# Kernel tuning notes

Measured on AMD Instinct MI355X. Metric: run time of the kernel, lower is better.

## Reference

```python
import jax, jax.numpy as jnp
import numpy as np

N_NODES = 100000


def gcn_conv(x, src, dst, W, b):
    # x: [N, F_in]; src/dst include self-loops; symmetric degree normalization (PyG GCNConv)
    n = x.shape[0]
    xw = x @ W  # [N, F_out]
    ones = jnp.ones(dst.shape[0], dtype=xw.dtype)
    deg = jax.ops.segment_sum(ones, dst, num_segments=n)  # in-degree incl. self-loop
    dinv = jnp.where(deg > 0, jax.lax.rsqrt(deg), 0.0)
    norm = dinv[src] * dinv[dst]  # [E]
    msg = xw[src] * norm[:, None]  # gather + per-edge scale
    out = jax.ops.segment_sum(msg, dst, num_segments=n)  # scatter-add aggregation
    return out + b


def setup_inputs() -> dict:
    key = jax.random.key(0)
    ks = jax.random.split(key, 6)
    F_in = 512
    E = 3200000
    x = jax.random.normal(ks[0], (N_NODES, F_in), dtype=jnp.float32)
    edge_index = jax.random.randint(ks[1], (2, E), 0, N_NODES, dtype=jnp.int64)
    W1 = jax.random.normal(ks[2], (F_in, 16), dtype=jnp.float32) * (1.0 / np.sqrt(F_in))
    b1 = jnp.zeros((16,), dtype=jnp.float32)
    W2 = jax.random.normal(ks[3], (16, 16), dtype=jnp.float32) * 0.25
    b2 = jnp.zeros((16,), dtype=jnp.float32)
    fc_w = jax.random.normal(ks[4], (16, 1), dtype=jnp.float32) * 0.25
    fc_b = jnp.zeros((1,), dtype=jnp.float32)
    return {"x": x, "edge_index": edge_index, "W1": W1, "b1": b1,
            "W2": W2, "b2": b2, "fc_w": fc_w, "fc_b": fc_b}


def reference(x, edge_index, W1, b1, W2, b2, fc_w, fc_b):
    n = x.shape[0]
    loop = jnp.arange(n, dtype=edge_index.dtype)
    src = jnp.concatenate([edge_index[0], loop])  # add self-loops
    dst = jnp.concatenate([edge_index[1], loop])
    h = jax.nn.relu(gcn_conv(x, src, dst, W1, b1))
    h = jax.nn.relu(gcn_conv(h, src, dst, W2, b2))
    g = jnp.mean(h, axis=0, keepdims=True)  # global_mean_pool, single graph -> [1, 16]
    return g @ fc_w + fc_b  # [1, 1]
```

## Files before the change

kernel.cpp:

```cpp
#include <hip/hip_runtime.h>
#include <stdint.h>

#define F_IN 512
#define F_OUT 16
#define CB_SHIFT 8
#define CB_W 256
#define PER 6250
#define SORT_CAP 6400

__device__ inline float4 f4_shfl_xor(float4 v, int mask) {
    float4 r;
    r.x = __shfl_xor(v.x, mask);
    r.y = __shfl_xor(v.y, mask);
    r.z = __shfl_xor(v.z, mask);
    r.w = __shfl_xor(v.w, mask);
    return r;
}

__global__ __launch_bounds__(256) void k_chist(const int* __restrict__ ei, int E, int K1, int B,
                                               int* __restrict__ cntT) {
    __shared__ int h[512];
    int t = threadIdx.x;
    for (int i = t; i < K1; i += 256) h[i] = 0;
    __syncthreads();
    int e0 = blockIdx.x * PER, e1 = min(E, e0 + PER);
    for (int e = e0 + t; e < e1; e += 256)
        atomicAdd(&h[ei[(size_t)E + e] >> CB_SHIFT], 1);
    __syncthreads();
    for (int i = t; i < K1; i += 256) cntT[(size_t)i * B + blockIdx.x] = h[i];
}

__global__ __launch_bounds__(512) void k_btot(const int* __restrict__ cntT, int B, int K1,
                                              int* __restrict__ bucketBase, int* __restrict__ bucketCnt) {
    __shared__ int sm[512];
    int k = threadIdx.x;
    int tot = 0;
    if (k < K1) {
        const int4* row = (const int4*)(cntT + (size_t)k * B);
        for (int b = 0; b < B / 4; b++) {
            int4 v = row[b];
            tot += v.x + v.y + v.z + v.w;
        }
    }
    sm[k] = tot;
    __syncthreads();
    for (int off = 1; off < 512; off <<= 1) {
        int add = (k >= off) ? sm[k - off] : 0;
        __syncthreads();
        sm[k] += add;
        __syncthreads();
    }
    if (k < K1) { bucketBase[k] = sm[k] - tot; bucketCnt[k] = tot; }
}

__global__ __launch_bounds__(512) void k_bbase(const int* __restrict__ cntT, int B,
                                               const int* __restrict__ bucketBase,
                                               int* __restrict__ baseT) {
    __shared__ int sm[512];
    int k = blockIdx.x, t = threadIdx.x;
    int v = (t < B) ? cntT[(size_t)k * B + t] : 0;
    sm[t] = v;
    __syncthreads();
    for (int off = 1; off < 512; off <<= 1) {
        int add = (t >= off) ? sm[t - off] : 0;
        __syncthreads();
        sm[t] += add;
        __syncthreads();
    }
    if (t < B) baseT[(size_t)k * B + t] = bucketBase[k] + sm[t] - v;
}

__global__ __launch_bounds__(512) void k_csort(const int* __restrict__ ei, int E, int K1, int B,
                                               const int* __restrict__ baseT, unsigned* __restrict__ part) {
    __shared__ unsigned sorted[SORT_CAP];
    __shared__ int h[512], lb[512], cur[512], gb[512];
    int t = threadIdx.x;
    int e0 = blockIdx.x * PER, e1 = min(E, e0 + PER);
    int C = e1 - e0;
    h[t] = 0;
    __syncthreads();
    for (int e = e0 + t; e < e1; e += 512)
        atomicAdd(&h[ei[(size_t)E + e] >> CB_SHIFT], 1);
    __syncthreads();
    int v = h[t];
    lb[t] = v;
    __syncthreads();
    for (int off = 1; off < 512; off <<= 1) {
        int add = (t >= off) ? lb[t - off] : 0;
        __syncthreads();
        lb[t] += add;
        __syncthreads();
    }
    int excl = lb[t] - v;
    __syncthreads();
    lb[t] = excl;
    cur[t] = excl;
    if (t < K1) gb[t] = baseT[(size_t)t * B + blockIdx.x];
    __syncthreads();
    for (int e = e0 + t; e < e1; e += 512) {
        int s = ei[e];
        int d = ei[(size_t)E + e];
        int pos = atomicAdd(&cur[d >> CB_SHIFT], 1);
        sorted[pos] = ((unsigned)s << CB_SHIFT) | (unsigned)(d & (CB_W - 1));
    }
    __syncthreads();
    int wv = t >> 6, ln = t & 63;
    for (int k = wv; k < K1; k += 8) {
        int s0 = lb[k];
        int s1 = cur[k];
        int g  = gb[k];
        for (int i = s0 + ln; i < s1; i += 64)
            part[(size_t)g + (i - s0)] = sorted[i];
    }
}

__global__ __launch_bounds__(512) void k_prep2(const unsigned* __restrict__ part,
                                               const int* __restrict__ bucketBase, const int* __restrict__ bucketCnt,
                                               int* __restrict__ hist, float* __restrict__ dinv,
                                               int* __restrict__ offsets, int* __restrict__ csr, int N) {
    __shared__ int fh[CB_W], fb[CB_W], cur[CB_W];
    int k = blockIdx.x, t = threadIdx.x;
    int base = bucketBase[k], cnt = bucketCnt[k];
    int d0 = k << CB_SHIFT;
    if (t < CB_W) fh[t] = 0;
    __syncthreads();
    for (int i = t; i < cnt; i += 512)
        atomicAdd(&fh[part[(size_t)base + i] & (CB_W - 1)], 1);
    __syncthreads();
    int v = 0;
    if (t < CB_W) { v = fh[t]; fb[t] = v; }
    __syncthreads();
    for (int off = 1; off < CB_W; off <<= 1) {
        int add = (t >= off && t < CB_W) ? fb[t - off] : 0;
        __syncthreads();
        if (t < CB_W) fb[t] += add;
        __syncthreads();
    }
    if (t < CB_W) {
        int excl = fb[t] - v;
        int n = d0 + t;
        if (n < N) {
            offsets[n] = base + excl;
            hist[n] = v;
            dinv[n] = rsqrtf((float)(v + 1));
        }
        cur[t] = excl;
    }
    __syncthreads();
    for (int i = t; i < cnt; i += 512) {
        unsigned e = part[(size_t)base + i];
        int pos = atomicAdd(&cur[e & (CB_W - 1)], 1);
        csr[(size_t)base + pos] = (int)(e >> CB_SHIFT);
    }
}

__global__ __launch_bounds__(128) void k_gemm1(const float* __restrict__ x, const float* __restrict__ W1,
                                               const float* __restrict__ dinv, float* __restrict__ xw1p, int N) {
    __shared__ float4 Wv[2048];
    const float4* w1v = (const float4*)W1;
    for (int i = threadIdx.x; i < 2048; i += 128) Wv[i] = w1v[i];
    __syncthreads();

    int t = threadIdx.x;
    int n0 = blockIdx.x * 256 + t;
    int n1 = n0 + 128;
    const float4* xr0 = (const float4*)(x + (size_t)min(n0, N - 1) * F_IN);
    const float4* xr1 = (const float4*)(x + (size_t)min(n1, N - 1) * F_IN);

    float acc0[16], acc1[16];
#pragma unroll
    for (int j = 0; j < 16; j++) { acc0[j] = 0.f; acc1[j] = 0.f; }

#pragma unroll 2
    for (int kk = 0; kk < 128; kk++) {
        float4 x0 = xr0[kk];
        float4 x1 = xr1[kk];
        const float4* wr = &Wv[kk * 16];
#pragma unroll
        for (int i = 0; i < 4; i++) {
            float xs0 = (i == 0) ? x0.x : (i == 1) ? x0.y : (i == 2) ? x0.z : x0.w;
            float xs1 = (i == 0) ? x1.x : (i == 1) ? x1.y : (i == 2) ? x1.z : x1.w;
#pragma unroll
            for (int q = 0; q < 4; q++) {
                float4 wv = wr[i * 4 + q];
                acc0[q*4+0] = fmaf(xs0, wv.x, acc0[q*4+0]);
                acc0[q*4+1] = fmaf(xs0, wv.y, acc0[q*4+1]);
                acc0[q*4+2] = fmaf(xs0, wv.z, acc0[q*4+2]);
                acc0[q*4+3] = fmaf(xs0, wv.w, acc0[q*4+3]);
                acc1[q*4+0] = fmaf(xs1, wv.x, acc1[q*4+0]);
                acc1[q*4+1] = fmaf(xs1, wv.y, acc1[q*4+1]);
                acc1[q*4+2] = fmaf(xs1, wv.z, acc1[q*4+2]);
                acc1[q*4+3] = fmaf(xs1, wv.w, acc1[q*4+3]);
            }
        }
    }
    if (n0 < N) {
        float dn = dinv[n0];
        float4* orow = (float4*)(xw1p + (size_t)n0 * F_OUT);
#pragma unroll
        for (int q = 0; q < 4; q++)
            orow[q] = make_float4(dn*acc0[q*4+0], dn*acc0[q*4+1], dn*acc0[q*4+2], dn*acc0[q*4+3]);
    }
    if (n1 < N) {
        float dn = dinv[n1];
        float4* orow = (float4*)(xw1p + (size_t)n1 * F_OUT);
#pragma unroll
        for (int q = 0; q < 4; q++)
            orow[q] = make_float4(dn*acc1[q*4+0], dn*acc1[q*4+1], dn*acc1[q*4+2], dn*acc1[q*4+3]);
    }
}

__global__ __launch_bounds__(256) void k_agg1(const float* __restrict__ xw, const int* __restrict__ offsets,
                                              const int* __restrict__ hist, const float* __restrict__ dinv,
                                              const int* __restrict__ csr, const float* __restrict__ b1,
                                              const float* __restrict__ W2, float* __restrict__ xw2p, int N) {
    __shared__ float W2s[256];
    if (threadIdx.x < 256) W2s[threadIdx.x] = W2[threadIdx.x];
    __syncthreads();

    int lane = threadIdx.x & 63;
    int wave = threadIdx.x >> 6;
    int grp  = lane >> 4;
    int sub  = lane & 15;
    int eo   = sub >> 2;
    int q    = sub & 3;
    int node = blockIdx.x * 16 + wave * 4 + grp;
    if (node >= N) return;

    int start = offsets[node], cnt = hist[node];
    float dn = dinv[node];
    float4 a0 = make_float4(0.f,0.f,0.f,0.f), a1 = a0, a2 = a0, a3 = a0;
    int i = 0;
    for (; i + 16 <= cnt; i += 16) {
        int s0 = csr[start + i + eo];
        int s1 = csr[start + i + 4 + eo];
        int s2 = csr[start + i + 8 + eo];
        int s3 = csr[start + i + 12 + eo];
        float4 v0 = ((const float4*)(xw + (size_t)s0 * F_OUT))[q];
        float4 v1 = ((const float4*)(xw + (size_t)s1 * F_OUT))[q];
        float4 v2 = ((const float4*)(xw + (size_t)s2 * F_OUT))[q];
        float4 v3 = ((const float4*)(xw + (size_t)s3 * F_OUT))[q];
        a0.x+=v0.x; a0.y+=v0.y; a0.z+=v0.z; a0.w+=v0.w;
        a1.x+=v1.x; a1.y+=v1.y; a1.z+=v1.z; a1.w+=v1.w;
        a2.x+=v2.x; a2.y+=v2.y; a2.z+=v2.z; a2.w+=v2.w;
        a3.x+=v3.x; a3.y+=v3.y; a3.z+=v3.z; a3.w+=v3.w;
    }
    for (; i + 8 <= cnt; i += 8) {
        int s0 = csr[start + i + eo];
        int s1 = csr[start + i + 4 + eo];
        float4 v0 = ((const float4*)(xw + (size_t)s0 * F_OUT))[q];
        float4 v1 = ((const float4*)(xw + (size_t)s1 * F_OUT))[q];
        a0.x+=v0.x; a0.y+=v0.y; a0.z+=v0.z; a0.w+=v0.w;
        a1.x+=v1.x; a1.y+=v1.y; a1.z+=v1.z; a1.w+=v1.w;
    }
    for (; i < cnt; i += 4) {
        if (i + eo < cnt) {
            int s0 = csr[start + i + eo];
            float4 v0 = ((const float4*)(xw + (size_t)s0 * F_OUT))[q];
            a0.x+=v0.x; a0.y+=v0.y; a0.z+=v0.z; a0.w+=v0.w;
        }
    }
    float4 acc;
    acc.x = a0.x+a1.x+a2.x+a3.x;
    acc.y = a0.y+a1.y+a2.y+a3.y;
    acc.z = a0.z+a1.z+a2.z+a3.z;
    acc.w = a0.w+a1.w+a2.w+a3.w;
    { float4 u = f4_shfl_xor(acc, 4); acc.x+=u.x; acc.y+=u.y; acc.z+=u.z; acc.w+=u.w; }
    { float4 u = f4_shfl_xor(acc, 8); acc.x+=u.x; acc.y+=u.y; acc.z+=u.z; acc.w+=u.w; }

    float4 sv = ((const float4*)(xw + (size_t)node * F_OUT))[q];
    float4 bq = ((const float4*)b1)[q];
    float4 h;
    h.x = fmaxf(dn * (acc.x + sv.x) + bq.x, 0.f);
    h.y = fmaxf(dn * (acc.y + sv.y) + bq.y, 0.f);
    h.z = fmaxf(dn * (acc.z + sv.z) + bq.z, 0.f);
    h.w = fmaxf(dn * (acc.w + sv.w) + bq.w, 0.f);

    float o = 0.f;
#pragma unroll
    for (int a = 0; a < 4; a++) {
        int src = (grp << 4) + a;
        float h0 = __shfl(h.x, src);
        float h1 = __shfl(h.y, src);
        float h2 = __shfl(h.z, src);
        float h3 = __shfl(h.w, src);
        o += h0 * W2s[(a*4+0)*16 + sub] + h1 * W2s[(a*4+1)*16 + sub]
           + h2 * W2s[(a*4+2)*16 + sub] + h3 * W2s[(a*4+3)*16 + sub];
    }
    xw2p[(size_t)node * F_OUT + sub] = dn * o;
}

__global__ __launch_bounds__(256) void k_agg2(const float* __restrict__ xw, const int* __restrict__ offsets,
                                              const int* __restrict__ hist, const float* __restrict__ dinv,
                                              const int* __restrict__ csr, const float* __restrict__ b2,
                                              float* __restrict__ partials, int N) {
    int lane = threadIdx.x & 63;
    int wave = threadIdx.x >> 6;
    int grp  = lane >> 4;
    int sub  = lane & 15;
    int eo   = sub >> 2;
    int q    = sub & 3;
    int node = blockIdx.x * 16 + wave * 4 + grp;

    float4 m = make_float4(0.f, 0.f, 0.f, 0.f);
    if (node < N) {
        int start = offsets[node], cnt = hist[node];
        float dn = dinv[node];
        float4 a0 = make_float4(0.f,0.f,0.f,0.f), a1 = a0, a2 = a0, a3 = a0;
        int i = 0;
        for (; i + 16 <= cnt; i += 16) {
            int s0 = csr[start + i + eo];
            int s1 = csr[start + i + 4 + eo];
            int s2 = csr[start + i + 8 + eo];
            int s3 = csr[start + i + 12 + eo];
            float4 v0 = ((const float4*)(xw + (size_t)s0 * F_OUT))[q];
            float4 v1 = ((const float4*)(xw + (size_t)s1 * F_OUT))[q];
            float4 v2 = ((const float4*)(xw + (size_t)s2 * F_OUT))[q];
            float4 v3 = ((const float4*)(xw + (size_t)s3 * F_OUT))[q];
            a0.x+=v0.x; a0.y+=v0.y; a0.z+=v0.z; a0.w+=v0.w;
            a1.x+=v1.x; a1.y+=v1.y; a1.z+=v1.z; a1.w+=v1.w;
            a2.x+=v2.x; a2.y+=v2.y; a2.z+=v2.z; a2.w+=v2.w;
            a3.x+=v3.x; a3.y+=v3.y; a3.z+=v3.z; a3.w+=v3.w;
        }
        for (; i + 8 <= cnt; i += 8) {
            int s0 = csr[start + i + eo];
            int s1 = csr[start + i + 4 + eo];
            float4 v0 = ((const float4*)(xw + (size_t)s0 * F_OUT))[q];
            float4 v1 = ((const float4*)(xw + (size_t)s1 * F_OUT))[q];
            a0.x+=v0.x; a0.y+=v0.y; a0.z+=v0.z; a0.w+=v0.w;
            a1.x+=v1.x; a1.y+=v1.y; a1.z+=v1.z; a1.w+=v1.w;
        }
        for (; i < cnt; i += 4) {
            if (i + eo < cnt) {
                int s0 = csr[start + i + eo];
                float4 v0 = ((const float4*)(xw + (size_t)s0 * F_OUT))[q];
                a0.x+=v0.x; a0.y+=v0.y; a0.z+=v0.z; a0.w+=v0.w;
            }
        }
        float4 acc;
        acc.x = a0.x+a1.x+a2.x+a3.x;
        acc.y = a0.y+a1.y+a2.y+a3.y;
        acc.z = a0.z+a1.z+a2.z+a3.z;
        acc.w = a0.w+a1.w+a2.w+a3.w;
        { float4 u = f4_shfl_xor(acc, 4); acc.x+=u.x; acc.y+=u.y; acc.z+=u.z; acc.w+=u.w; }
        { float4 u = f4_shfl_xor(acc, 8); acc.x+=u.x; acc.y+=u.y; acc.z+=u.z; acc.w+=u.w; }
        float4 sv = ((const float4*)(xw + (size_t)node * F_OUT))[q];
        float4 bq = ((const float4*)b2)[q];
        if (eo == 0) {
            m.x = fmaxf(dn * (acc.x + sv.x) + bq.x, 0.f);
            m.y = fmaxf(dn * (acc.y + sv.y) + bq.y, 0.f);
            m.z = fmaxf(dn * (acc.z + sv.z) + bq.z, 0.f);
            m.w = fmaxf(dn * (acc.w + sv.w) + bq.w, 0.f);
        }
    }
    { float4 u = f4_shfl_xor(m, 16); m.x+=u.x; m.y+=u.y; m.z+=u.z; m.w+=u.w; }
    { float4 u = f4_shfl_xor(m, 32); m.x+=u.x; m.y+=u.y; m.z+=u.z; m.w+=u.w; }
    __shared__ float smf[4][16];
    if (lane < 4) {
        smf[wave][q*4+0] = m.x;
        smf[wave][q*4+1] = m.y;
        smf[wave][q*4+2] = m.z;
        smf[wave][q*4+3] = m.w;
    }
    __syncthreads();
    if (threadIdx.x < 16) {
        float s = smf[0][threadIdx.x] + smf[1][threadIdx.x] + smf[2][threadIdx.x] + smf[3][threadIdx.x];
        partials[(size_t)blockIdx.x * 16 + threadIdx.x] = s;
    }
}

__global__ void k_final(const float* __restrict__ partials, int NB, const float* __restrict__ fc_w,
                        const float* __restrict__ fc_b, float* __restrict__ out, float invN) {
    __shared__ float sm[64][16];
    int t = threadIdx.x;
    int g = t >> 4, j = t & 15;
    float s = 0.0f;
    for (int bk = g; bk < NB; bk += 64) s += partials[(size_t)bk * 16 + j];
    sm[g][j] = s;
    __syncthreads();
    for (int str = 32; str > 0; str >>= 1) {
        if (g < str) sm[g][j] += sm[g + str][j];
        __syncthreads();
    }
    if (t == 0) {
        float acc = fc_b[0];
#pragma unroll
        for (int jj = 0; jj < 16; jj++) acc += sm[0][jj] * invN * fc_w[jj];
        out[0] = acc;
    }
}

extern "C" void kernel_launch(void* const* d_in, const int* in_sizes, int n_in,
                              void* d_out, int out_size, void* d_ws, size_t ws_size,
                              hipStream_t stream) {
    const float* x   = (const float*)d_in[0];
    const int*   ei  = (const int*)d_in[1];
    const float* W1  = (const float*)d_in[2];
    const float* b1  = (const float*)d_in[3];
    const float* W2  = (const float*)d_in[4];
    const float* b2  = (const float*)d_in[5];
    const float* fcw = (const float*)d_in[6];
    const float* fcb = (const float*)d_in[7];
    float* out = (float*)d_out;

    int N = in_sizes[0] / F_IN;
    int E = in_sizes[1] / 2;
    int K1 = (N + CB_W - 1) >> CB_SHIFT;
    int B1 = (E + PER - 1) / PER;

    char* p = (char*)d_ws;
    auto alloc = [&](size_t bytes) {
        void* r = (void*)p;
        p += (bytes + 255) & ~(size_t)255;
        return r;
    };
    int*   cntT       = (int*)alloc((size_t)K1 * B1 * 4);
    int*   baseT      = (int*)alloc((size_t)K1 * B1 * 4);
    int*   bucketBase = (int*)alloc((size_t)K1 * 4);
    int*   bucketCnt  = (int*)alloc((size_t)K1 * 4);
    int*   hist       = (int*)alloc((size_t)N * 4);
    int*   offsets    = (int*)alloc((size_t)N * 4);
    float* dinv       = (float*)alloc((size_t)N * 4);
    int*   csr        = (int*)alloc((size_t)E * 4);
    unsigned* part    = (unsigned*)alloc((size_t)E * 4);
    int NB_NODE = (N + 15) / 16;
    float* partials = (float*)alloc((size_t)NB_NODE * 16 * 4);
    float* xw1p = (float*)part;
    float* xw2p = xw1p + (size_t)N * F_OUT;

    k_chist<<<B1, 256, 0, stream>>>(ei, E, K1, B1, cntT);
    k_btot<<<1, 512, 0, stream>>>(cntT, B1, K1, bucketBase, bucketCnt);
    k_bbase<<<K1, 512, 0, stream>>>(cntT, B1, bucketBase, baseT);
    k_csort<<<B1, 512, 0, stream>>>(ei, E, K1, B1, baseT, part);
    k_prep2<<<K1, 512, 0, stream>>>(part, bucketBase, bucketCnt, hist, dinv, offsets, csr, N);

    k_gemm1<<<(N + 255) / 256, 128, 0, stream>>>(x, W1, dinv, xw1p, N);
    k_agg1<<<NB_NODE, 256, 0, stream>>>(xw1p, offsets, hist, dinv, csr, b1, W2, xw2p, N);
    k_agg2<<<NB_NODE, 256, 0, stream>>>(xw2p, offsets, hist, dinv, csr, b2, partials, N);
    k_final<<<1, 1024, 0, stream>>>(partials, NB_NODE, fcw, fcb, out, 1.0f / (float)N);
}
```

Baseline: 258.6 us.

## Simplify GEMM1 to one row per thread, widen csort copy groups, deepen agg unroll

The first-layer GEMM now gives each of 256 threads a single row and reads W1 directly from global memory (uniform addresses, likely scalar or broadcast loads) instead of staging it in LDS with two rows per thread. The csort scatter-out loop uses 16-lane groups per bucket instead of whole 64-lane waves, which suits short per-bucket runs. Both aggregation kernels gain a 32-edge unrolled loop so each lane has eight independent gathers in flight. The changes trade LDS reuse and per-thread work for more threads and memory-level parallelism, at some cost in register pressure.

```diff
diff --git a/kernel.cpp b/kernel.cpp
--- a/kernel.cpp
+++ b/kernel.cpp
@@ -76,7 +76,6 @@
     __shared__ int h[512], lb[512], cur[512], gb[512];
     int t = threadIdx.x;
     int e0 = blockIdx.x * PER, e1 = min(E, e0 + PER);
-    int C = e1 - e0;
     h[t] = 0;
     __syncthreads();
     for (int e = e0 + t; e < e1; e += 512)
@@ -104,12 +103,12 @@
         sorted[pos] = ((unsigned)s << CB_SHIFT) | (unsigned)(d & (CB_W - 1));
     }
     __syncthreads();
-    int wv = t >> 6, ln = t & 63;
-    for (int k = wv; k < K1; k += 8) {
+    int g16 = t >> 4, ln = t & 15;
+    for (int k = g16; k < K1; k += 32) {
         int s0 = lb[k];
         int s1 = cur[k];
         int g  = gb[k];
-        for (int i = s0 + ln; i < s1; i += 64)
+        for (int i = s0 + ln; i < s1; i += 16)
             part[(size_t)g + (i - s0)] = sorted[i];
     }
 }
@@ -154,60 +153,38 @@
     }
 }
 
-__global__ __launch_bounds__(128) void k_gemm1(const float* __restrict__ x, const float* __restrict__ W1,
+__global__ __launch_bounds__(256) void k_gemm1(const float* __restrict__ x, const float* __restrict__ W1,
                                                const float* __restrict__ dinv, float* __restrict__ xw1p, int N) {
-    __shared__ float4 Wv[2048];
-    const float4* w1v = (const float4*)W1;
-    for (int i = threadIdx.x; i < 2048; i += 128) Wv[i] = w1v[i];
-    __syncthreads();
-
-    int t = threadIdx.x;
-    int n0 = blockIdx.x * 256 + t;
-    int n1 = n0 + 128;
-    const float4* xr0 = (const float4*)(x + (size_t)min(n0, N - 1) * F_IN);
-    const float4* xr1 = (const float4*)(x + (size_t)min(n1, N - 1) * F_IN);
-
-    float acc0[16], acc1[16];
-#pragma unroll
-    for (int j = 0; j < 16; j++) { acc0[j] = 0.f; acc1[j] = 0.f; }
-
-#pragma unroll 2
+    int n = blockIdx.x * 256 + threadIdx.x;
+    if (n >= N) return;
+    const float4* xr = (const float4*)(x + (size_t)n * F_IN);
+    const float4* wr = (const float4*)W1;
+
+    float acc[16];
+#pragma unroll
+    for (int j = 0; j < 16; j++) acc[j] = 0.f;
+
+#pragma unroll 4
     for (int kk = 0; kk < 128; kk++) {
-        float4 x0 = xr0[kk];
-        float4 x1 = xr1[kk];
-        const float4* wr = &Wv[kk * 16];
+        float4 xv = xr[kk];
 #pragma unroll
         for (int i = 0; i < 4; i++) {
-            float xs0 = (i == 0) ? x0.x : (i == 1) ? x0.y : (i == 2) ? x0.z : x0.w;
-            float xs1 = (i == 0) ? x1.x : (i == 1) ? x1.y : (i == 2) ? x1.z : x1.w;
+            float xs = (i == 0) ? xv.x : (i == 1) ? xv.y : (i == 2) ? xv.z : xv.w;
 #pragma unroll
             for (int q = 0; q < 4; q++) {
-                float4 wv = wr[i * 4 + q];
-                acc0[q*4+0] = fmaf(xs0, wv.x, acc0[q*4+0]);
-                acc0[q*4+1] = fmaf(xs0, wv.y, acc0[q*4+1]);
-                acc0[q*4+2] = fmaf(xs0, wv.z, acc0[q*4+2]);
-                acc0[q*4+3] = fmaf(xs0, wv.w, acc0[q*4+3]);
-                acc1[q*4+0] = fmaf(xs1, wv.x, acc1[q*4+0]);
-                acc1[q*4+1] = fmaf(xs1, wv.y, acc1[q*4+1]);
-                acc1[q*4+2] = fmaf(xs1, wv.z, acc1[q*4+2]);
-                acc1[q*4+3] = fmaf(xs1, wv.w, acc1[q*4+3]);
+                float4 wv = wr[kk * 16 + i * 4 + q];
+                acc[q*4+0] = fmaf(xs, wv.x, acc[q*4+0]);
+                acc[q*4+1] = fmaf(xs, wv.y, acc[q*4+1]);
+                acc[q*4+2] = fmaf(xs, wv.z, acc[q*4+2]);
+                acc[q*4+3] = fmaf(xs, wv.w, acc[q*4+3]);
             }
         }
     }
-    if (n0 < N) {
-        float dn = dinv[n0];
-        float4* orow = (float4*)(xw1p + (size_t)n0 * F_OUT);
-#pragma unroll
-        for (int q = 0; q < 4; q++)
-            orow[q] = make_float4(dn*acc0[q*4+0], dn*acc0[q*4+1], dn*acc0[q*4+2], dn*acc0[q*4+3]);
-    }
-    if (n1 < N) {
-        float dn = dinv[n1];
-        float4* orow = (float4*)(xw1p + (size_t)n1 * F_OUT);
-#pragma unroll
-        for (int q = 0; q < 4; q++)
-            orow[q] = make_float4(dn*acc1[q*4+0], dn*acc1[q*4+1], dn*acc1[q*4+2], dn*acc1[q*4+3]);
-    }
+    float dn = dinv[n];
+    float4* orow = (float4*)(xw1p + (size_t)n * F_OUT);
+#pragma unroll
+    for (int q = 0; q < 4; q++)
+        orow[q] = make_float4(dn*acc[q*4+0], dn*acc[q*4+1], dn*acc[q*4+2], dn*acc[q*4+3]);
 }
 
 __global__ __launch_bounds__(256) void k_agg1(const float* __restrict__ xw, const int* __restrict__ offsets,
@@ -231,6 +208,32 @@
     float dn = dinv[node];
     float4 a0 = make_float4(0.f,0.f,0.f,0.f), a1 = a0, a2 = a0, a3 = a0;
     int i = 0;
+    for (; i + 32 <= cnt; i += 32) {
+        int s0 = csr[start + i + eo];
+        int s1 = csr[start + i + 4 + eo];
+        int s2 = csr[start + i + 8 + eo];
+        int s3 = csr[start + i + 12 + eo];
+        int s4 = csr[start + i + 16 + eo];
+        int s5 = csr[start + i + 20 + eo];
+        int s6 = csr[start + i + 24 + eo];
+        int s7 = csr[start + i + 28 + eo];
+        float4 v0 = ((const float4*)(xw + (size_t)s0 * F_OUT))[q];
+        float4 v1 = ((const float4*)(xw + (size_t)s1 * F_OUT))[q];
+        float4 v2 = ((const float4*)(xw + (size_t)s2 * F_OUT))[q];
+        float4 v3 = ((const float4*)(xw + (size_t)s3 * F_OUT))[q];
+        float4 v4 = ((const float4*)(xw + (size_t)s4 * F_OUT))[q];
+        float4 v5 = ((const float4*)(xw + (size_t)s5 * F_OUT))[q];
+        float4 v6 = ((const float4*)(xw + (size_t)s6 * F_OUT))[q];
+        float4 v7 = ((const float4*)(xw + (size_t)s7 * F_OUT))[q];
+        a0.x+=v0.x; a0.y+=v0.y; a0.z+=v0.z; a0.w+=v0.w;
+        a1.x+=v1.x; a1.y+=v1.y; a1.z+=v1.z; a1.w+=v1.w;
+        a2.x+=v2.x; a2.y+=v2.y; a2.z+=v2.z; a2.w+=v2.w;
+        a3.x+=v3.x; a3.y+=v3.y; a3.z+=v3.z; a3.w+=v3.w;
+        a0.x+=v4.x; a0.y+=v4.y; a0.z+=v4.z; a0.w+=v4.w;
+        a1.x+=v5.x; a1.y+=v5.y; a1.z+=v5.z; a1.w+=v5.w;
+        a2.x+=v6.x; a2.y+=v6.y; a2.z+=v6.z; a2.w+=v6.w;
+        a3.x+=v7.x; a3.y+=v7.y; a3.z+=v7.z; a3.w+=v7.w;
+    }
     for (; i + 16 <= cnt; i += 16) {
         int s0 = csr[start + i + eo];
         int s1 = csr[start + i + 4 + eo];
@@ -308,6 +311,32 @@
         float dn = dinv[node];
         float4 a0 = make_float4(0.f,0.f,0.f,0.f), a1 = a0, a2 = a0, a3 = a0;
         int i = 0;
+        for (; i + 32 <= cnt; i += 32) {
+            int s0 = csr[start + i + eo];
+            int s1 = csr[start + i + 4 + eo];
+            int s2 = csr[start + i + 8 + eo];
+            int s3 = csr[start + i + 12 + eo];
+            int s4 = csr[start + i + 16 + eo];
+            int s5 = csr[start + i + 20 + eo];
+            int s6 = csr[start + i + 24 + eo];
+            int s7 = csr[start + i + 28 + eo];
+            float4 v0 = ((const float4*)(xw + (size_t)s0 * F_OUT))[q];
+            float4 v1 = ((const float4*)(xw + (size_t)s1 * F_OUT))[q];
+            float4 v2 = ((const float4*)(xw + (size_t)s2 * F_OUT))[q];
+            float4 v3 = ((const float4*)(xw + (size_t)s3 * F_OUT))[q];
+            float4 v4 = ((const float4*)(xw + (size_t)s4 * F_OUT))[q];
+            float4 v5 = ((const float4*)(xw + (size_t)s5 * F_OUT))[q];
+            float4 v6 = ((const float4*)(xw + (size_t)s6 * F_OUT))[q];
+            float4 v7 = ((const float4*)(xw + (size_t)s7 * F_OUT))[q];
+            a0.x+=v0.x; a0.y+=v0.y; a0.z+=v0.z; a0.w+=v0.w;
+            a1.x+=v1.x; a1.y+=v1.y; a1.z+=v1.z; a1.w+=v1.w;
+            a2.x+=v2.x; a2.y+=v2.y; a2.z+=v2.z; a2.w+=v2.w;
+            a3.x+=v3.x; a3.y+=v3.y; a3.z+=v3.z; a3.w+=v3.w;
+            a0.x+=v4.x; a0.y+=v4.y; a0.z+=v4.z; a0.w+=v4.w;
+            a1.x+=v5.x; a1.y+=v5.y; a1.z+=v5.z; a1.w+=v5.w;
+            a2.x+=v6.x; a2.y+=v6.y; a2.z+=v6.z; a2.w+=v6.w;
+            a3.x+=v7.x; a3.y+=v7.y; a3.z+=v7.z; a3.w+=v7.w;
+        }
         for (; i + 16 <= cnt; i += 16) {
             int s0 = csr[start + i + eo];
             int s1 = csr[start + i + 4 + eo];
@@ -434,7 +463,7 @@
     k_csort<<<B1, 512, 0, stream>>>(ei, E, K1, B1, baseT, part);
     k_prep2<<<K1, 512, 0, stream>>>(part, bucketBase, bucketCnt, hist, dinv, offsets, csr, N);
 
-    k_gemm1<<<(N + 255) / 256, 128, 0, stream>>>(x, W1, dinv, xw1p, N);
+    k_gemm1<<<(N + 255) / 256, 256, 0, stream>>>(x, W1, dinv, xw1p, N);
     k_agg1<<<NB_NODE, 256, 0, stream>>>(xw1p, offsets, hist, dinv, csr, b1, W2, xw2p, N);
     k_agg2<<<NB_NODE, 256, 0, stream>>>(xw2p, offsets, hist, dinv, csr, b2, partials, N);
     k_final<<<1, 1024, 0, stream>>>(partials, NB_NODE, fcw, fcb, out, 1.0f / (float)N);
```

Result: faster. 237.0 us (-8.3%).
